# Optimization experiments

Measured on AMD Instinct MI355X. Metric: run time of the kernel, lower is better.

The kernel has to match this reference:

```python
import jax, jax.numpy as jnp
import numpy as np

B, T, E, NH = 2, 2048, 512, 8
HD = E // NH
SCALE = float(HD) ** -0.5


def setup_inputs() -> dict:
    key = jax.random.key(0)
    ks = jax.random.split(key, 7)
    s = 0.02
    return {
        "x": jax.random.normal(ks[0], (B, T, E), dtype=jnp.float32),
        "w_qkv": jax.random.normal(ks[1], (E, 3 * E), dtype=jnp.float32) * s,
        "b_qkv": jax.random.normal(ks[2], (3 * E,), dtype=jnp.float32) * s,
        "w_od": jax.random.normal(ks[3], (E, 2 * NH), dtype=jnp.float32) * s,
        "b_od": jax.random.normal(ks[4], (2 * NH,), dtype=jnp.float32) * s,
        "w_out": jax.random.normal(ks[5], (E, E), dtype=jnp.float32) * s,
        "b_out": jax.random.normal(ks[6], (E,), dtype=jnp.float32) * s,
    }


def _heads(t):  # (B,T,E) -> (B*NH, T, HD)
    return t.reshape(B, T, NH, HD).transpose(0, 2, 1, 3).reshape(B * NH, T, HD)


def _point_mask(idx, j):  # idx: (B*NH,T) float indices -> one-hot (B*NH,T,T)
    return (j[None, None, :] == idx[:, :, None]).astype(jnp.float32)


def reference(x, w_qkv, b_qkv, w_od, b_od, w_out, b_out):
    qkv = x @ w_qkv + b_qkv
    Q, K, V = jnp.split(qkv, 3, axis=-1)  # each (B,T,E)

    od = Q @ w_od + b_od  # (B,T,2*NH)
    offset, duration = jnp.split(od, 2, axis=-1)
    offset = jnp.tanh(offset) * T
    duration = jax.nn.sigmoid(duration) * T

    query_index = jnp.arange(T, dtype=x.dtype)[None, :, None]  # (1,T,1)
    anchor = query_index + offset  # (B,T,NH)
    # 'b t nh -> (b nh) t'
    anchor = anchor.transpose(0, 2, 1).reshape(B * NH, T)
    duration = duration.transpose(0, 2, 1).reshape(B * NH, T)

    start = anchor - duration
    end = anchor + duration
    bound_l = jnp.floor(start)
    bound_r = jnp.ceil(end)
    anchor_l = jnp.floor(anchor)
    anchor_r = anchor_l + 1.0

    j = jnp.arange(T, dtype=x.dtype)
    neg_bound_weight = (bound_l - start)[:, :, None] * _point_mask(bound_l, j) \
                     + (end - bound_r)[:, :, None] * _point_mask(bound_r, j)
    anchor_dist_l = anchor - anchor_l
    anchor_weight = anchor_dist_l[:, :, None] * _point_mask(anchor_r, j) \
                  + (1.0 - anchor_dist_l)[:, :, None] * _point_mask(anchor_l, j)
    point_weight = 1.0 + neg_bound_weight + anchor_weight  # (B*NH,T,T)

    # segment mask: True OUTSIDE [bound_l, bound_r]
    attn_mask = (j[None, None, :] < bound_l[:, :, None]) | (j[None, None, :] > bound_r[:, :, None])

    Qh, Kh, Vh = _heads(Q), _heads(K), _heads(V)  # (B*NH, T, HD)
    scores = jnp.einsum('bic,brc->bir', Qh, Kh) * SCALE * point_weight
    scores = jnp.where(attn_mask, jnp.asarray(-1e8, scores.dtype), scores)
    attn = jax.nn.softmax(scores, axis=-1)
    out = jnp.einsum('bir,brc->bic', attn, Vh)  # (B*NH,T,HD)
    out = out.reshape(B, NH, T, HD).transpose(0, 2, 1, 3).reshape(B, T, E)
    return out @ w_out + b_out
```

## Files before the change

### kernel.cpp

```cpp
#include <hip/hip_runtime.h>
#include <math.h>

typedef float vf4 __attribute__((ext_vector_type(4)));
typedef float f32x4 __attribute__((ext_vector_type(4)));
typedef short bf16x8 __attribute__((ext_vector_type(8)));
typedef short short4v __attribute__((ext_vector_type(4)));
typedef int int2v __attribute__((ext_vector_type(2)));
typedef int int4v __attribute__((ext_vector_type(4)));

constexpr int B = 2, T = 2048, E = 512, NH = 8, HD = 64;
constexpr int BH = B * NH;
constexpr int NT = BH * T;
constexpr int KSPLIT = 4;
constexpr float SCALE = 0.125f;
constexpr float LOG2E = 1.44269504088896f;
constexpr float QSC = SCALE * LOG2E;

static __device__ __forceinline__ short f2bf(float f) {
  unsigned u = __float_as_uint(f);
  unsigned r = (u + 0x7fffu + ((u >> 16) & 1u)) >> 16;
  return (short)r;
}
static __device__ __forceinline__ unsigned pk2bf(float a, float b) {
  unsigned lo = (unsigned)(unsigned short)f2bf(a);
  unsigned hi = (unsigned)(unsigned short)f2bf(b);
  return lo | (hi << 16);
}
static __device__ __forceinline__ unsigned pkhu(float a, float b) {
  unsigned ua = __float_as_uint(a) + 0x8000u;
  unsigned ub = __float_as_uint(b) + 0x8000u;
  return __builtin_amdgcn_perm(ub, ua, 0x07060302u);
}
#if __has_builtin(__builtin_amdgcn_exp2f)
#define EXP2F(x) __builtin_amdgcn_exp2f(x)
#else
#define EXP2F(x) exp2f(x)
#endif
static __device__ __forceinline__ float bf2f(short s) {
  return __uint_as_float(((unsigned)(unsigned short)s) << 16);
}

__global__ __launch_bounds__(256) void prep_all(
    const float* __restrict__ x, const float* __restrict__ w_qkv,
    const float* __restrict__ b_qkv, const float* __restrict__ w_od,
    const float* __restrict__ b_od,
    short* __restrict__ xb, short* __restrict__ wTq, short* __restrict__ wTo,
    const float* __restrict__ w_out, float* __restrict__ Wc,
    float* __restrict__ bc)
{
  __shared__ float sh[8464];
  const int bid = blockIdx.x;
  const int tid = threadIdx.x;

  if (bid < 2048) {
    int idx = (bid * 256 + tid) * 4;
    vf4 v = *(const vf4*)&x[idx];
    short4v o;
    o[0] = f2bf(v[0]); o[1] = f2bf(v[1]); o[2] = f2bf(v[2]); o[3] = f2bf(v[3]);
    *(short4v*)&xb[idx] = o;
  } else if (bid < 3072) {
    const float* w; short* wT; int N, t;
    if (bid < 2816) { t = bid - 2048; w = w_qkv; wT = wTq; N = 1536; }
    else            { t = bid - 2816; w = w_out; wT = wTo; N = 512; }
    float (*tt)[33] = (float(*)[33])sh;
    const int k0 = (t & 15) * 32;
    const int n0 = (t >> 4) * 32;
    const int c = tid & 31, r = tid >> 5;
#pragma unroll
    for (int p = 0; p < 4; ++p)
      tt[r + p * 8][c] = w[(size_t)(k0 + r + p * 8) * N + n0 + c];
    __syncthreads();
#pragma unroll
    for (int p = 0; p < 4; ++p)
      wT[(size_t)(n0 + r + p * 8) * 512 + k0 + c] = f2bf(tt[c][r + p * 8]);
  } else {
    float* Lod = sh;
    float (*pb)[17] = (float(*)[17])(sh + 8192);
    const int bx = bid - 3072;
#pragma unroll
    for (int p = 0; p < 8; ++p) {
      int idx = (p * 256 + tid) * 4;
      *(vf4*)&Lod[idx] = *(const vf4*)&w_od[idx];
    }
    __syncthreads();
    if (bx < 32) {
      const int k = bx * 16 + (tid >> 4);
      const int c = tid & 15;
      float s = 0.0f;
      for (int m = 0; m < E; m += 4) {
        vf4 wq = *(const vf4*)&w_qkv[(size_t)k * 1536 + m];
        s += wq[0] * Lod[(m + 0) * 16 + c] + wq[1] * Lod[(m + 1) * 16 + c]
           + wq[2] * Lod[(m + 2) * 16 + c] + wq[3] * Lod[(m + 3) * 16 + c];
      }
      Wc[k * 16 + c] = s;
    } else {
      const int c = tid & 15, seg = tid >> 4;
      float s = 0.0f;
      for (int m = seg * 32; m < seg * 32 + 32; ++m)
        s += b_qkv[m] * Lod[m * 16 + c];
      pb[seg][c] = s;
      __syncthreads();
      if (tid < 16) {
        float acc = b_od[tid];
#pragma unroll
        for (int g = 0; g < 16; ++g) acc += pb[g][tid];
        bc[tid] = acc;
      }
    }
  }
}

__global__ __launch_bounds__(256) void qkv_od(
    const short* __restrict__ xb, const short* __restrict__ wT,
    const float* __restrict__ bias, short* __restrict__ qkvb,
    short* __restrict__ Vtg,
    const float* __restrict__ x, const float* __restrict__ Wc,
    const float* __restrict__ bc, float* __restrict__ prm)
{
  __shared__ __align__(16) short smem_s[16896];
  const int bid = blockIdx.x;
  const int tid = threadIdx.x;

  if (bid < 768) {
    short* As = smem_s;
    short* Bt = smem_s + 128 * 40;
    const int wave = tid >> 6, lane = tid & 63;
    const int quad = lane >> 4, l15 = lane & 15;
    const int wm = wave >> 1, wn = wave & 1;
    const int bx = bid % 24, by = bid / 24;
    const int m0 = by * 128, n0 = bx * 64;

    f32x4 acc[4][2];
#pragma unroll
    for (int mi = 0; mi < 4; ++mi)
#pragma unroll
      for (int ni = 0; ni < 2; ++ni) acc[mi][ni] = (f32x4){0, 0, 0, 0};

    const int sr = tid >> 1, sc = (tid & 1) * 16;
    const int br2 = tid >> 2, bk2 = (tid & 3) * 8;

#pragma unroll 1
    for (int k0 = 0; k0 < E; k0 += 32) {
      __syncthreads();
      *(bf16x8*)&As[sr * 40 + sc] =
          *(const bf16x8*)&xb[(size_t)(m0 + sr) * 512 + k0 + sc];
      *(bf16x8*)&As[sr * 40 + sc + 8] =
          *(const bf16x8*)&xb[(size_t)(m0 + sr) * 512 + k0 + sc + 8];
      *(bf16x8*)&Bt[br2 * 40 + bk2] =
          *(const bf16x8*)&wT[(size_t)(n0 + br2) * 512 + k0 + bk2];
      __syncthreads();

      bf16x8 aA[4], bB[2];
#pragma unroll
      for (int mi = 0; mi < 4; ++mi)
        aA[mi] = *(const bf16x8*)&As[(wm * 64 + mi * 16 + l15) * 40 + quad * 8];
#pragma unroll
      for (int ni = 0; ni < 2; ++ni)
        bB[ni] = *(const bf16x8*)&Bt[(wn * 32 + ni * 16 + l15) * 40 + quad * 8];
#pragma unroll
      for (int mi = 0; mi < 4; ++mi)
#pragma unroll
        for (int ni = 0; ni < 2; ++ni)
          acc[mi][ni] = __builtin_amdgcn_mfma_f32_16x16x32_bf16(
              aA[mi], bB[ni], acc[mi][ni], 0, 0, 0);
    }

#pragma unroll
    for (int mi = 0; mi < 4; ++mi)
#pragma unroll
      for (int ni = 0; ni < 2; ++ni) {
        const int col = n0 + wn * 32 + ni * 16 + l15;
        const int rowb = m0 + wm * 64 + mi * 16 + quad * 4;
        const float bs = bias[col];
        if (col < 1024) {
          const float qs = (col < 512) ? QSC : 1.0f;
#pragma unroll
          for (int r = 0; r < 4; ++r)
            qkvb[(size_t)(rowb + r) * 1536 + col] =
                f2bf((acc[mi][ni][r] + bs) * qs);
        } else {
          const int h = (col - 1024) >> 6, hd = col & 63;
          const int b = rowb >> 11, tt = rowb & 2047;
          int2v pk;
          pk[0] = (int)pk2bf(acc[mi][ni][0] + bs, acc[mi][ni][1] + bs);
          pk[1] = (int)pk2bf(acc[mi][ni][2] + bs, acc[mi][ni][3] + bs);
          *(int2v*)&Vtg[(size_t)(((b << 3) + h) * 64 + hd) * T + tt] = pk;
        }
      }
  } else {
    float* Lod = (float*)smem_s;
    float* ods = ((float*)smem_s) + 8192;
    const int obx = bid - 768;
#pragma unroll
    for (int p = 0; p < 8; ++p) {
      int idx = (p * 256 + tid) * 4;
      *(vf4*)&Lod[idx] = *(const vf4*)&Wc[idx];
    }
    __syncthreads();

    const int r = tid >> 4, c = tid & 15;
    const int row = obx * 16 + r;
    float sum = bc[c];
    const float* qr = x + (size_t)row * E;
    for (int k = 0; k < E; k += 4) {
      vf4 q = *(const vf4*)&qr[k];
      sum += q[0] * Lod[(k + 0) * 16 + c]
           + q[1] * Lod[(k + 1) * 16 + c]
           + q[2] * Lod[(k + 2) * 16 + c]
           + q[3] * Lod[(k + 3) * 16 + c];
    }
    ods[r * 16 + c] = sum;
    __syncthreads();

    if (tid < 128) {
      const int rr = tid >> 3, h = tid & 7;
      const int grow = obx * 16 + rr;
      const int b = grow / T, i = grow % T;
      float o = ods[rr * 16 + h];
      float d = ods[rr * 16 + h + 8];
      float offset   = tanhf(o) * (float)T;
      float duration = (float)T / (1.0f + expf(-d));
      float anchor = (float)i + offset;
      float start = anchor - duration;
      float end   = anchor + duration;
      float bl = floorf(start);
      float br = ceilf(end);
      float al = floorf(anchor);
      float wbl = bl - start;
      float wbr = end - br;
      float af  = anchor - al;
      float rsc = 1.0f;
      if (br < 0.0f || bl > (float)(T - 1)) {
        bl = 0.0f; br = (float)(T - 1);
        wbl = 0.0f; wbr = 0.0f; al = -5.0f; af = 0.0f;
        rsc = 0.0f;
      }
      int idx = (b * NH + h) * T + i;
      prm[0 * NT + idx] = bl;
      prm[1 * NT + idx] = br;
      prm[2 * NT + idx] = wbl;
      prm[3 * NT + idx] = wbr;
      prm[4 * NT + idx] = al;
      prm[5 * NT + idx] = af;
      prm[6 * NT + idx] = rsc;
    }
  }
}

__global__ __launch_bounds__(256, 4) void flash_attn_mfma5(
    const short* __restrict__ qkvb, const short* __restrict__ Vtg,
    const float* __restrict__ prm,
    short* __restrict__ Opart, float* __restrict__ lpart)
{
  __shared__ __align__(16) short Ks[2][64 * 72];
  __shared__ __align__(16) short Vt[2][64 * 72];
  __shared__ __align__(16) short Ps[4][16 * 72];
  __shared__ float u_s[8];

  const int tid = threadIdx.x;
  const int wave = tid >> 6, lane = tid & 63;
  const int quad = lane >> 4, l15 = lane & 15;
  const int qt = blockIdx.x, bh = blockIdx.y, ks = blockIdx.z;
  const int b = bh >> 3, h = bh & 7;
  const int i0 = qt * 64;
  const int i = i0 + wave * 16 + l15;

  const int pidx = bh * T + i;
  float blf = prm[0 * NT + pidx];
  float brf = prm[1 * NT + pidx];
  float wbl = prm[2 * NT + pidx];
  float wbr = prm[3 * NT + pidx];
  float alf = prm[4 * NT + pidx];
  float afr = prm[5 * NT + pidx];
  float rsc = prm[6 * NT + pidx];
  const int bli = (int)blf, widi = (int)brf - bli, ali = (int)alf;
  const unsigned widu = (unsigned)widi;
  const float a1 = 1.0f - afr;

  bf16x8 aQ0, aQ1;
  {
    size_t bq = (size_t)(b * T + i) * 1536 + h * 64;
    aQ0 = *(const bf16x8*)&qkvb[bq + quad * 8];
    aQ1 = *(const bf16x8*)&qkvb[bq + 32 + quad * 8];
    if (rsc == 0.0f) {
      bf16x8 z = {0, 0, 0, 0, 0, 0, 0, 0};
      aQ0 = z; aQ1 = z;
    }
  }

  float bmn = blf, bmx = brf;
#pragma unroll
  for (int d = 1; d < 64; d <<= 1) {
    bmn = fminf(bmn, __shfl_xor(bmn, d));
    bmx = fmaxf(bmx, __shfl_xor(bmx, d));
  }
  if (lane == 0) { u_s[wave * 2] = bmn; u_s[wave * 2 + 1] = bmx; }
  __syncthreads();
  bmn = fminf(fminf(u_s[0], u_s[2]), fminf(u_s[4], u_s[6]));
  bmx = fmaxf(fmaxf(u_s[1], u_s[3]), fmaxf(u_s[5], u_s[7]));
  const int ktlo = max(ks * 8, max(((int)bmn) >> 6, 0));
  const int kthi = min(ks * 8 + 7, min(((int)bmx) >> 6, T / 64 - 1));

  f32x4 o[4];
#pragma unroll
  for (int c = 0; c < 4; ++c) o[c] = (f32x4){0, 0, 0, 0};
  float lacc = 0.0f;

  const int rq = tid >> 3, cb = (tid & 7) * 8;
  const short* kbase = qkvb + (size_t)b * T * 1536 + 512 + h * 64 + cb;
  const short* vbase = Vtg + (size_t)bh * 64 * T + cb;

  bf16x8 kr0, kr1, vr0, vr1;
  if (ktlo <= kthi) {
    const int j0 = ktlo * 64;
    kr0 = *(const bf16x8*)&kbase[(size_t)(j0 + rq) * 1536];
    kr1 = *(const bf16x8*)&kbase[(size_t)(j0 + 32 + rq) * 1536];
    vr0 = *(const bf16x8*)&vbase[(size_t)rq * T + j0];
    vr1 = *(const bf16x8*)&vbase[(size_t)(32 + rq) * T + j0];
    *(bf16x8*)&Ks[0][rq * 72 + cb] = kr0;
    *(bf16x8*)&Ks[0][(32 + rq) * 72 + cb] = kr1;
    *(bf16x8*)&Vt[0][rq * 72 + cb] = vr0;
    *(bf16x8*)&Vt[0][(32 + rq) * 72 + cb] = vr1;
  }
  __syncthreads();

  int buf = 0;
#pragma unroll 1
  for (int kt = ktlo; kt <= kthi; ++kt) {
    const int j0 = kt * 64;
    if (kt < kthi) {
      const int j1 = j0 + 64;
      kr0 = *(const bf16x8*)&kbase[(size_t)(j1 + rq) * 1536];
      kr1 = *(const bf16x8*)&kbase[(size_t)(j1 + 32 + rq) * 1536];
      vr0 = *(const bf16x8*)&vbase[(size_t)rq * T + j1];
      vr1 = *(const bf16x8*)&vbase[(size_t)(32 + rq) * T + j1];
    }

    const short* KsB = Ks[buf];
    const short* VtB = Vt[buf];

    f32x4 s[4];
#pragma unroll
    for (int nc = 0; nc < 4; ++nc) {
      const short* kb = &KsB[(nc * 16 + l15) * 72 + quad * 8];
      f32x4 a = (f32x4){0, 0, 0, 0};
      a = __builtin_amdgcn_mfma_f32_16x16x32_bf16(*(const bf16x8*)&kb[0],  aQ0, a, 0, 0, 0);
      a = __builtin_amdgcn_mfma_f32_16x16x32_bf16(*(const bf16x8*)&kb[32], aQ1, a, 0, 0, 0);
      s[nc] = a;
    }

    const int clean = (bli < j0) & (bli + widi > j0 + 63) &
                      ((ali > j0 + 63) | (ali + 1 < j0));
    if (__all(clean)) {
#pragma unroll
      for (int nc = 0; nc < 4; ++nc) {
        float p0 = EXP2F(s[nc][0]);
        float p1 = EXP2F(s[nc][1]);
        float p2 = EXP2F(s[nc][2]);
        float p3 = EXP2F(s[nc][3]);
        lacc += (p0 + p1) + (p2 + p3);
        int2v pk;
        pk[0] = (int)pkhu(p0, p1);
        pk[1] = (int)pkhu(p2, p3);
        *(int2v*)&Ps[wave][l15 * 72 + nc * 16 + quad * 4] = pk;
      }
    } else {
      const int dq  = j0 + quad * 4 - bli;
      const int dq2 = j0 + quad * 4 - ali;
#pragma unroll
      for (int nc = 0; nc < 4; ++nc) {
        const int dn = dq + nc * 16, d2n = dq2 + nc * 16;
        float pr[4];
#pragma unroll
        for (int r = 0; r < 4; ++r) {
          int d = dn + r, d2 = d2n + r;
          float e  = (d == 0) ? wbl : ((d == widi) ? wbr : 0.0f);
          float aw = (d2 == 0) ? a1 : ((d2 == 1) ? afr : 0.0f);
          float w = 1.0f + e + aw;
          float v = s[nc][r] * w;
          v = ((unsigned)d <= widu) ? v : -115.0f;
          float p = EXP2F(v);
          lacc += p;
          pr[r] = p;
        }
        int2v pk;
        pk[0] = (int)pkhu(pr[0], pr[1]);
        pk[1] = (int)pkhu(pr[2], pr[3]);
        *(int2v*)&Ps[wave][l15 * 72 + nc * 16 + quad * 4] = pk;
      }
    }

    bf16x8 bP0 = *(const bf16x8*)&Ps[wave][l15 * 72 + quad * 8];
    bf16x8 bP1 = *(const bf16x8*)&Ps[wave][l15 * 72 + 32 + quad * 8];
#pragma unroll
    for (int nc2 = 0; nc2 < 4; ++nc2) {
      const short* vb = &VtB[(nc2 * 16 + l15) * 72 + quad * 8];
      o[nc2] = __builtin_amdgcn_mfma_f32_16x16x32_bf16(
          *(const bf16x8*)&vb[0],  bP0, o[nc2], 0, 0, 0);
      o[nc2] = __builtin_amdgcn_mfma_f32_16x16x32_bf16(
          *(const bf16x8*)&vb[32], bP1, o[nc2], 0, 0, 0);
    }

    if (kt < kthi) {
      short* Kn = Ks[buf ^ 1];
      short* Vn = Vt[buf ^ 1];
      *(bf16x8*)&Kn[rq * 72 + cb] = kr0;
      *(bf16x8*)&Kn[(32 + rq) * 72 + cb] = kr1;
      *(bf16x8*)&Vn[rq * 72 + cb] = vr0;
      *(bf16x8*)&Vn[(32 + rq) * 72 + cb] = vr1;
      __syncthreads();
      buf ^= 1;
    }
  }

  lacc += __shfl_xor(lacc, 16);
  lacc += __shfl_xor(lacc, 32);
  if (lane < 16)
    lpart[ks * NT + bh * T + i] = lacc;

  size_t ob = (size_t)ks * (B * T * E) + (size_t)(b * T + i) * E + h * 64;
#pragma unroll
  for (int nc2 = 0; nc2 < 4; ++nc2) {
    int2v pk;
    pk[0] = (int)pk2bf(o[nc2][0], o[nc2][1]);
    pk[1] = (int)pk2bf(o[nc2][2], o[nc2][3]);
    *(int2v*)&Opart[ob + nc2 * 16 + quad * 4] = pk;
  }
}

__global__ __launch_bounds__(256) void combine_attn(
    const short* __restrict__ Opart, const float* __restrict__ lpart,
    short* __restrict__ attnb)
{
  int base = (blockIdx.x * 256 + threadIdx.x) * 8;
  int row = base >> 9;
  int c = base & 511;
  int h = c >> 6;
  int b = row >> 11;
  int i = row & (T - 1);
  int lidx = ((b << 3) + h) * T + i;
  float l = (lpart[lidx] + lpart[NT + lidx]) +
            (lpart[2 * NT + lidx] + lpart[3 * NT + lidx]);
  float inv = 1.0f / l;
  bf16x8 o0 = *(const bf16x8*)&Opart[base];
  bf16x8 o1 = *(const bf16x8*)&Opart[(size_t)(B * T * E) + base];
  bf16x8 o2 = *(const bf16x8*)&Opart[(size_t)(2 * B * T * E) + base];
  bf16x8 o3 = *(const bf16x8*)&Opart[(size_t)(3 * B * T * E) + base];
  int4v ov;
#pragma unroll
  for (int j = 0; j < 4; ++j) {
    float a = ((bf2f(o0[2 * j]) + bf2f(o1[2 * j])) +
               (bf2f(o2[2 * j]) + bf2f(o3[2 * j]))) * inv;
    float bb = ((bf2f(o0[2 * j + 1]) + bf2f(o1[2 * j + 1])) +
                (bf2f(o2[2 * j + 1]) + bf2f(o3[2 * j + 1]))) * inv;
    ov[j] = (int)pk2bf(a, bb);
  }
  *(int4v*)&attnb[base] = ov;
}

__global__ __launch_bounds__(256) void out_gemm_bf16(
    const short* __restrict__ Ab, const short* __restrict__ wT,
    const float* __restrict__ bias, float* __restrict__ Co)
{
  __shared__ __align__(16) short As[64 * 40];
  __shared__ __align__(16) short Bt[64 * 40];

  const int tid = threadIdx.x;
  const int wave = tid >> 6, lane = tid & 63;
  const int quad = lane >> 4, l15 = lane & 15;
  const int wm = wave >> 1, wn = wave & 1;
  const int m0 = blockIdx.y * 64, n0 = blockIdx.x * 64;

  f32x4 acc[2][2];
#pragma unroll
  for (int mi = 0; mi < 2; ++mi)
#pragma unroll
    for (int ni = 0; ni < 2; ++ni) acc[mi][ni] = (f32x4){0, 0, 0, 0};

  const int ar = tid >> 2, akc = (tid & 3) * 8;

#pragma unroll 1
  for (int k0 = 0; k0 < E; k0 += 32) {
    __syncthreads();
    *(bf16x8*)&As[ar * 40 + akc] =
        *(const bf16x8*)&Ab[(size_t)(m0 + ar) * 512 + k0 + akc];
    *(bf16x8*)&Bt[ar * 40 + akc] =
        *(const bf16x8*)&wT[(size_t)(n0 + ar) * 512 + k0 + akc];
    __syncthreads();

    bf16x8 aA[2], bB[2];
#pragma unroll
    for (int mi = 0; mi < 2; ++mi)
      aA[mi] = *(const bf16x8*)&As[(wm * 32 + mi * 16 + l15) * 40 + quad * 8];
#pragma unroll
    for (int ni = 0; ni < 2; ++ni)
      bB[ni] = *(const bf16x8*)&Bt[(wn * 32 + ni * 16 + l15) * 40 + quad * 8];
#pragma unroll
    for (int mi = 0; mi < 2; ++mi)
#pragma unroll
      for (int ni = 0; ni < 2; ++ni)
        acc[mi][ni] = __builtin_amdgcn_mfma_f32_16x16x32_bf16(
            aA[mi], bB[ni], acc[mi][ni], 0, 0, 0);
  }

#pragma unroll
  for (int mi = 0; mi < 2; ++mi)
#pragma unroll
    for (int ni = 0; ni < 2; ++ni)
#pragma unroll
      for (int r = 0; r < 4; ++r) {
        int row = m0 + wm * 32 + mi * 16 + quad * 4 + r;
        int col = n0 + wn * 32 + ni * 16 + l15;
        Co[(size_t)row * 512 + col] = acc[mi][ni][r] + bias[col];
      }
}

extern "C" void kernel_launch(void* const* d_in, const int* in_sizes, int n_in,
                              void* d_out, int out_size, void* d_ws, size_t ws_size,
                              hipStream_t stream)
{
  const float* x     = (const float*)d_in[0];
  const float* w_qkv = (const float*)d_in[1];
  const float* b_qkv = (const float*)d_in[2];
  const float* w_od  = (const float*)d_in[3];
  const float* b_od  = (const float*)d_in[4];
  const float* w_out = (const float*)d_in[5];
  const float* b_out = (const float*)d_in[6];
  float* out = (float*)d_out;

  char* w = (char*)d_ws;
  short* xb    = (short*)w;  w += (size_t)B * T * E * 2;
  short* wTq   = (short*)w;  w += (size_t)E * 3 * E * 2;
  short* wTo   = (short*)w;  w += (size_t)E * E * 2;
  short* qkvb  = (short*)w;  w += (size_t)B * T * 3 * E * 2;
  short* Vtg   = (short*)w;  w += (size_t)B * T * E * 2;
  float* Wc    = (float*)w;  w += (size_t)E * 16 * 4;
  float* bc    = (float*)w;  w += 256;
  float* prm   = (float*)w;  w += (size_t)7 * NT * 4;
  short* Opart = (short*)w;  w += (size_t)KSPLIT * B * T * E * 2;
  float* lpart = (float*)w;  w += (size_t)KSPLIT * NT * 4;
  short* attnb = (short*)w;  w += (size_t)B * T * E * 2;

  prep_all<<<dim3(3105), 256, 0, stream>>>(
      x, w_qkv, b_qkv, w_od, b_od, xb, wTq, wTo, w_out, Wc, bc);

  qkv_od<<<dim3(1024), 256, 0, stream>>>(
      xb, wTq, b_qkv, qkvb, Vtg, x, Wc, bc, prm);

  flash_attn_mfma5<<<dim3(T / 64, BH, KSPLIT), 256, 0, stream>>>(
      qkvb, Vtg, prm, Opart, lpart);

  combine_attn<<<dim3(B * T * E / 2048), 256, 0, stream>>>(Opart, lpart, attnb);

  out_gemm_bf16<<<dim3(E / 64, B * T / 64), 256, 0, stream>>>(
      attnb, wTo, b_out, out);
}
```

Baseline: 163.6 us.

## Double-buffer GEMM tiles with deeper prefetch and compute row sums via MFMA

The QKV and output GEMM K-loops now use two LDS buffers with register prefetch two stages ahead, which halves the barriers per tile and overlaps global loads with MFMA work. The flash-attention loop is unrolled by two and prefetches K/V two tiles ahead using two register sets. The softmax denominator is now accumulated with an extra MFMA against a ones vector instead of per-lane scalar adds and shuffles. This raises register and LDS use, which may lower occupancy, and the row sum is now taken from the bf16-rounded probabilities.

```diff
diff --git a/kernel.cpp b/kernel.cpp
--- a/kernel.cpp
+++ b/kernel.cpp
@@ -122,8 +122,6 @@
   const int tid = threadIdx.x;
 
   if (bid < 768) {
-    short* As = smem_s;
-    short* Bt = smem_s + 128 * 40;
     const int wave = tid >> 6, lane = tid & 63;
     const int quad = lane >> 4, l15 = lane & 15;
     const int wm = wave >> 1, wn = wave & 1;
@@ -139,31 +137,49 @@
     const int sr = tid >> 1, sc = (tid & 1) * 16;
     const int br2 = tid >> 2, bk2 = (tid & 3) * 8;
 
+#define QLD(R, K0) do {                                                   \
+      R[0] = *(const bf16x8*)&xb[(size_t)(m0 + sr) * 512 + (K0) + sc];    \
+      R[1] = *(const bf16x8*)&xb[(size_t)(m0 + sr) * 512 + (K0) + sc + 8];\
+      R[2] = *(const bf16x8*)&wT[(size_t)(n0 + br2) * 512 + (K0) + bk2];  \
+    } while (0)
+#define QST(BUF, R) do {                                                  \
+      short* As_ = smem_s + (BUF) * 7680;                                 \
+      short* Bt_ = As_ + 5120;                                            \
+      *(bf16x8*)&As_[sr * 40 + sc] = R[0];                                \
+      *(bf16x8*)&As_[sr * 40 + sc + 8] = R[1];                            \
+      *(bf16x8*)&Bt_[br2 * 40 + bk2] = R[2];                              \
+    } while (0)
+#define QMM(BUF) do {                                                     \
+      const short* As_ = smem_s + (BUF) * 7680;                           \
+      const short* Bt_ = As_ + 5120;                                      \
+      bf16x8 aA[4], bB[2];                                                \
+      for (int mi = 0; mi < 4; ++mi)                                      \
+        aA[mi] = *(const bf16x8*)&As_[(wm * 64 + mi * 16 + l15) * 40 + quad * 8]; \
+      for (int ni = 0; ni < 2; ++ni)                                      \
+        bB[ni] = *(const bf16x8*)&Bt_[(wn * 32 + ni * 16 + l15) * 40 + quad * 8]; \
+      for (int mi = 0; mi < 4; ++mi)                                      \
+        for (int ni = 0; ni < 2; ++ni)                                    \
+          acc[mi][ni] = __builtin_amdgcn_mfma_f32_16x16x32_bf16(          \
+              aA[mi], bB[ni], acc[mi][ni], 0, 0, 0);                      \
+    } while (0)
+
+    bf16x8 rA[3], rB[3];
+    QLD(rA, 0); QST(0, rA);
+    QLD(rA, 32);
+    __syncthreads();
 #pragma unroll 1
-    for (int k0 = 0; k0 < E; k0 += 32) {
+    for (int k0 = 0; k0 < 512; k0 += 64) {
+      if (k0 + 64 < 512) QLD(rB, k0 + 64);
+      QMM(0);
+      QST(1, rA);
       __syncthreads();
-      *(bf16x8*)&As[sr * 40 + sc] =
-          *(const bf16x8*)&xb[(size_t)(m0 + sr) * 512 + k0 + sc];
-      *(bf16x8*)&As[sr * 40 + sc + 8] =
-          *(const bf16x8*)&xb[(size_t)(m0 + sr) * 512 + k0 + sc + 8];
-      *(bf16x8*)&Bt[br2 * 40 + bk2] =
-          *(const bf16x8*)&wT[(size_t)(n0 + br2) * 512 + k0 + bk2];
-      __syncthreads();
-
-      bf16x8 aA[4], bB[2];
-#pragma unroll
-      for (int mi = 0; mi < 4; ++mi)
-        aA[mi] = *(const bf16x8*)&As[(wm * 64 + mi * 16 + l15) * 40 + quad * 8];
-#pragma unroll
-      for (int ni = 0; ni < 2; ++ni)
-        bB[ni] = *(const bf16x8*)&Bt[(wn * 32 + ni * 16 + l15) * 40 + quad * 8];
-#pragma unroll
-      for (int mi = 0; mi < 4; ++mi)
-#pragma unroll
-        for (int ni = 0; ni < 2; ++ni)
-          acc[mi][ni] = __builtin_amdgcn_mfma_f32_16x16x32_bf16(
-              aA[mi], bB[ni], acc[mi][ni], 0, 0, 0);
-    }
+      if (k0 + 96 < 512) QLD(rA, k0 + 96);
+      QMM(1);
+      if (k0 + 64 < 512) { QST(0, rB); __syncthreads(); }
+    }
+#undef QLD
+#undef QST
+#undef QMM
 
 #pragma unroll
     for (int mi = 0; mi < 4; ++mi)
@@ -247,7 +263,7 @@
   }
 }
 
-__global__ __launch_bounds__(256, 4) void flash_attn_mfma5(
+__global__ __launch_bounds__(256, 4) void flash_attn_mfma6(
     const short* __restrict__ qkvb, const short* __restrict__ Vtg,
     const float* __restrict__ prm,
     short* __restrict__ Opart, float* __restrict__ lpart)
@@ -304,40 +320,31 @@
   f32x4 o[4];
 #pragma unroll
   for (int c = 0; c < 4; ++c) o[c] = (f32x4){0, 0, 0, 0};
-  float lacc = 0.0f;
+  f32x4 lq = (f32x4){0, 0, 0, 0};
+  const short BF1 = (short)0x3F80;
+  const bf16x8 vone = {BF1, BF1, BF1, BF1, BF1, BF1, BF1, BF1};
 
   const int rq = tid >> 3, cb = (tid & 7) * 8;
   const short* kbase = qkvb + (size_t)b * T * 1536 + 512 + h * 64 + cb;
   const short* vbase = Vtg + (size_t)bh * 64 * T + cb;
 
-  bf16x8 kr0, kr1, vr0, vr1;
-  if (ktlo <= kthi) {
-    const int j0 = ktlo * 64;
-    kr0 = *(const bf16x8*)&kbase[(size_t)(j0 + rq) * 1536];
-    kr1 = *(const bf16x8*)&kbase[(size_t)(j0 + 32 + rq) * 1536];
-    vr0 = *(const bf16x8*)&vbase[(size_t)rq * T + j0];
-    vr1 = *(const bf16x8*)&vbase[(size_t)(32 + rq) * T + j0];
-    *(bf16x8*)&Ks[0][rq * 72 + cb] = kr0;
-    *(bf16x8*)&Ks[0][(32 + rq) * 72 + cb] = kr1;
-    *(bf16x8*)&Vt[0][rq * 72 + cb] = vr0;
-    *(bf16x8*)&Vt[0][(32 + rq) * 72 + cb] = vr1;
-  }
-  __syncthreads();
-
-  int buf = 0;
-#pragma unroll 1
-  for (int kt = ktlo; kt <= kthi; ++kt) {
-    const int j0 = kt * 64;
-    if (kt < kthi) {
-      const int j1 = j0 + 64;
-      kr0 = *(const bf16x8*)&kbase[(size_t)(j1 + rq) * 1536];
-      kr1 = *(const bf16x8*)&kbase[(size_t)(j1 + 32 + rq) * 1536];
-      vr0 = *(const bf16x8*)&vbase[(size_t)rq * T + j1];
-      vr1 = *(const bf16x8*)&vbase[(size_t)(32 + rq) * T + j1];
-    }
-
-    const short* KsB = Ks[buf];
-    const short* VtB = Vt[buf];
+#define FLD(R, KT) do { int j_ = (KT) * 64;                              \
+    R[0] = *(const bf16x8*)&kbase[(size_t)(j_ + rq) * 1536];             \
+    R[1] = *(const bf16x8*)&kbase[(size_t)(j_ + 32 + rq) * 1536];        \
+    R[2] = *(const bf16x8*)&vbase[(size_t)rq * T + j_];                  \
+    R[3] = *(const bf16x8*)&vbase[(size_t)(32 + rq) * T + j_];           \
+  } while (0)
+#define FST(BUF, R) do {                                                 \
+    *(bf16x8*)&Ks[BUF][rq * 72 + cb] = R[0];                             \
+    *(bf16x8*)&Ks[BUF][(32 + rq) * 72 + cb] = R[1];                      \
+    *(bf16x8*)&Vt[BUF][rq * 72 + cb] = R[2];                             \
+    *(bf16x8*)&Vt[BUF][(32 + rq) * 72 + cb] = R[3];                      \
+  } while (0)
+
+  auto compute = [&](int bufc, int ktc) {
+    const int j0 = ktc * 64;
+    const short* KsB = Ks[bufc];
+    const short* VtB = Vt[bufc];
 
     f32x4 s[4];
 #pragma unroll
@@ -358,7 +365,6 @@
         float p1 = EXP2F(s[nc][1]);
         float p2 = EXP2F(s[nc][2]);
         float p3 = EXP2F(s[nc][3]);
-        lacc += (p0 + p1) + (p2 + p3);
         int2v pk;
         pk[0] = (int)pkhu(p0, p1);
         pk[1] = (int)pkhu(p2, p3);
@@ -379,9 +385,7 @@
           float w = 1.0f + e + aw;
           float v = s[nc][r] * w;
           v = ((unsigned)d <= widu) ? v : -115.0f;
-          float p = EXP2F(v);
-          lacc += p;
-          pr[r] = p;
+          pr[r] = EXP2F(v);
         }
         int2v pk;
         pk[0] = (int)pkhu(pr[0], pr[1]);
@@ -392,6 +396,8 @@
 
     bf16x8 bP0 = *(const bf16x8*)&Ps[wave][l15 * 72 + quad * 8];
     bf16x8 bP1 = *(const bf16x8*)&Ps[wave][l15 * 72 + 32 + quad * 8];
+    lq = __builtin_amdgcn_mfma_f32_16x16x32_bf16(vone, bP0, lq, 0, 0, 0);
+    lq = __builtin_amdgcn_mfma_f32_16x16x32_bf16(vone, bP1, lq, 0, 0, 0);
 #pragma unroll
     for (int nc2 = 0; nc2 < 4; ++nc2) {
       const short* vb = &VtB[(nc2 * 16 + l15) * 72 + quad * 8];
@@ -400,23 +406,35 @@
       o[nc2] = __builtin_amdgcn_mfma_f32_16x16x32_bf16(
           *(const bf16x8*)&vb[32], bP1, o[nc2], 0, 0, 0);
     }
-
-    if (kt < kthi) {
-      short* Kn = Ks[buf ^ 1];
-      short* Vn = Vt[buf ^ 1];
-      *(bf16x8*)&Kn[rq * 72 + cb] = kr0;
-      *(bf16x8*)&Kn[(32 + rq) * 72 + cb] = kr1;
-      *(bf16x8*)&Vn[rq * 72 + cb] = vr0;
-      *(bf16x8*)&Vn[(32 + rq) * 72 + cb] = vr1;
+  };
+
+  if (ktlo <= kthi) {
+    bf16x8 rA[4], rB[4];
+    FLD(rA, ktlo);
+    FST(0, rA);
+    if (ktlo + 1 <= kthi) FLD(rA, ktlo + 1);
+    __syncthreads();
+    int buf = 0, kt = ktlo;
+    while (true) {
+      if (kt + 2 <= kthi) FLD(rB, kt + 2);
+      compute(buf, kt);
+      if (kt == kthi) break;
+      FST(buf ^ 1, rA);
       __syncthreads();
-      buf ^= 1;
-    }
-  }
-
-  lacc += __shfl_xor(lacc, 16);
-  lacc += __shfl_xor(lacc, 32);
+      buf ^= 1; ++kt;
+      if (kt + 2 <= kthi) FLD(rA, kt + 2);
+      compute(buf, kt);
+      if (kt == kthi) break;
+      FST(buf ^ 1, rB);
+      __syncthreads();
+      buf ^= 1; ++kt;
+    }
+  }
+#undef FLD
+#undef FST
+
   if (lane < 16)
-    lpart[ks * NT + bh * T + i] = lacc;
+    lpart[ks * NT + bh * T + i] = lq[0];
 
   size_t ob = (size_t)ks * (B * T * E) + (size_t)(b * T + i) * E + h * 64;
 #pragma unroll
@@ -462,8 +480,7 @@
     const short* __restrict__ Ab, const short* __restrict__ wT,
     const float* __restrict__ bias, float* __restrict__ Co)
 {
-  __shared__ __align__(16) short As[64 * 40];
-  __shared__ __align__(16) short Bt[64 * 40];
+  __shared__ __align__(16) short smem_o[10240];
 
   const int tid = threadIdx.x;
   const int wave = tid >> 6, lane = tid & 63;
@@ -479,29 +496,47 @@
 
   const int ar = tid >> 2, akc = (tid & 3) * 8;
 
+#define OLD(R, K0) do {                                                  \
+    R[0] = *(const bf16x8*)&Ab[(size_t)(m0 + ar) * 512 + (K0) + akc];    \
+    R[1] = *(const bf16x8*)&wT[(size_t)(n0 + ar) * 512 + (K0) + akc];    \
+  } while (0)
+#define OST(BUF, R) do {                                                 \
+    short* As_ = smem_o + (BUF) * 5120;                                  \
+    short* Bt_ = As_ + 2560;                                             \
+    *(bf16x8*)&As_[ar * 40 + akc] = R[0];                                \
+    *(bf16x8*)&Bt_[ar * 40 + akc] = R[1];                                \
+  } while (0)
+#define OMM(BUF) do {                                                    \
+    const short* As_ = smem_o + (BUF) * 5120;                            \
+    const short* Bt_ = As_ + 2560;                                       \
+    bf16x8 aA[2], bB[2];                                                 \
+    for (int mi = 0; mi < 2; ++mi)                                       \
+      aA[mi] = *(const bf16x8*)&As_[(wm * 32 + mi * 16 + l15) * 40 + quad * 8]; \
+    for (int ni = 0; ni < 2; ++ni)                                       \
+      bB[ni] = *(const bf16x8*)&Bt_[(wn * 32 + ni * 16 + l15) * 40 + quad * 8]; \
+    for (int mi = 0; mi < 2; ++mi)                                       \
+      for (int ni = 0; ni < 2; ++ni)                                     \
+        acc[mi][ni] = __builtin_amdgcn_mfma_f32_16x16x32_bf16(           \
+            aA[mi], bB[ni], acc[mi][ni], 0, 0, 0);                       \
+  } while (0)
+
+  bf16x8 rA[2], rB[2];
+  OLD(rA, 0); OST(0, rA);
+  OLD(rA, 32);
+  __syncthreads();
 #pragma unroll 1
-  for (int k0 = 0; k0 < E; k0 += 32) {
-    __syncthreads();
-    *(bf16x8*)&As[ar * 40 + akc] =
-        *(const bf16x8*)&Ab[(size_t)(m0 + ar) * 512 + k0 + akc];
-    *(bf16x8*)&Bt[ar * 40 + akc] =
-        *(const bf16x8*)&wT[(size_t)(n0 + ar) * 512 + k0 + akc];
-    __syncthreads();
-
-    bf16x8 aA[2], bB[2];
-#pragma unroll
-    for (int mi = 0; mi < 2; ++mi)
-      aA[mi] = *(const bf16x8*)&As[(wm * 32 + mi * 16 + l15) * 40 + quad * 8];
-#pragma unroll
-    for (int ni = 0; ni < 2; ++ni)
-      bB[ni] = *(const bf16x8*)&Bt[(wn * 32 + ni * 16 + l15) * 40 + quad * 8];
-#pragma unroll
-    for (int mi = 0; mi < 2; ++mi)
-#pragma unroll
-      for (int ni = 0; ni < 2; ++ni)
-        acc[mi][ni] = __builtin_amdgcn_mfma_f32_16x16x32_bf16(
-            aA[mi], bB[ni], acc[mi][ni], 0, 0, 0);
-  }
+  for (int k0 = 0; k0 < 512; k0 += 64) {
+    if (k0 + 64 < 512) OLD(rB, k0 + 64);
+    OMM(0);
+    OST(1, rA);
+    __syncthreads();
+    if (k0 + 96 < 512) OLD(rA, k0 + 96);
+    OMM(1);
+    if (k0 + 64 < 512) { OST(0, rB); __syncthreads(); }
+  }
+#undef OLD
+#undef OST
+#undef OMM
 
 #pragma unroll
   for (int mi = 0; mi < 2; ++mi)
@@ -547,7 +582,7 @@
   qkv_od<<<dim3(1024), 256, 0, stream>>>(
       xb, wTq, b_qkv, qkvb, Vtg, x, Wc, bc, prm);
 
-  flash_attn_mfma5<<<dim3(T / 64, BH, KSPLIT), 256, 0, stream>>>(
+  flash_attn_mfma6<<<dim3(T / 64, BH, KSPLIT), 256, 0, stream>>>(
       qkvb, Vtg, prm, Opart, lpart);
 
   combine_attn<<<dim3(B * T * E / 2048), 256, 0, stream>>>(Opart, lpart, attnb);
```

Result: slower. 203.0 us (+24.1%).
